# Optimization experiments

Hardware: AMD Instinct MI355X
Metric: run time of the kernel (lower is better)

## Reference

```python
import jax, jax.numpy as jnp
import numpy as np

R = 10000   # relation_num
E = 256     # emb_size == hidden_size
B = 1024    # batch
L = 8       # body length (loop runs L-1 steps)


def setup_inputs() -> dict:
    key = jax.random.key(0)
    ks = jax.random.split(key, 10)
    s = 0.05
    return {
        "bodys": jax.random.randint(ks[0], (B, L), 0, R),
        "emb_w": jax.random.normal(ks[1], (R, E), jnp.float32) * s,
        "w_ih": jax.random.normal(ks[2], (4 * E, E), jnp.float32) * s,
        "w_hh": jax.random.normal(ks[3], (4 * E, E), jnp.float32) * s,
        "b_ih": jax.random.normal(ks[4], (4 * E,), jnp.float32) * s,
        "b_hh": jax.random.normal(ks[5], (4 * E,), jnp.float32) * s,
        "fc1_w": jax.random.normal(ks[6], (E, 2 * E), jnp.float32) * s,
        "fc1_b": jax.random.normal(ks[7], (E,), jnp.float32) * s,
        "fc2_w": jax.random.normal(ks[8], (R + 1, E), jnp.float32) * s,
        "fc2_b": jax.random.normal(ks[9], (R + 1,), jnp.float32) * s,
    }


def _lstm(x, w_ih, w_hh, b_ih, b_hh):
    # x: [B, L, E] -> hidden states [B, L, H] (torch gate order i,f,g,o)
    Bn, _, H = x.shape[0], x.shape[1], w_hh.shape[1]
    h0 = jnp.zeros((Bn, H), x.dtype)
    c0 = jnp.zeros((Bn, H), x.dtype)

    def step(carry, xt):
        h, c = carry
        g = xt @ w_ih.T + b_ih + h @ w_hh.T + b_hh
        i, f, gg, o = jnp.split(g, 4, axis=-1)
        c = jax.nn.sigmoid(f) * c + jax.nn.sigmoid(i) * jnp.tanh(gg)
        h = jax.nn.sigmoid(o) * jnp.tanh(c)
        return (h, c), h

    _, hs = jax.lax.scan(step, (h0, c0), x.transpose(1, 0, 2))
    return hs.transpose(1, 0, 2)


def reference(bodys, emb_w, w_ih, w_hh, b_ih, b_hh, fc1_w, fc1_b, fc2_w, fc2_b):
    x = emb_w[bodys]                       # [B, L, E] embedded body relations
    body_hid = _lstm(x, w_ih, w_hh, b_ih, b_hh)  # [B, L, E]
    Rn = emb_w.shape[0]
    prob = emb_concat = prob_sf = None
    for i in range(body_hid.shape[1] - 1):   # short fixed unroll (L-1 steps)
        if i == 0:
            emb_1 = x[:, 0, :]
            second = x[:, 1, :]
        else:
            # prob_sf @ cat(embedding(indices), body_hid[:, i])  without [B,R+1,E]
            emb_1 = prob_sf[:, :Rn] @ emb_w + prob_sf[:, Rn:] * body_hid[:, i, :]
            # relation_emb[:, i+1, :] == emb_w[i+1] broadcast over batch
            second = jnp.broadcast_to(emb_w[i + 1], emb_1.shape)
        emb_concat = jnp.concatenate([emb_1, second], axis=1)   # [B, 2E]
        prob = jax.nn.relu(emb_concat @ fc1_w.T + fc1_b) @ fc2_w.T + fc2_b  # [B, R+1]
        prob_sf = jax.nn.softmax(prob, axis=1)
    return prob, emb_concat
```

## Files before the change

kernel.cpp:

```cpp
#include <hip/hip_runtime.h>

#define Bv 1024
#define Ev 256
#define Lv 8
#define Rv 10000
#define NP1 10001
#define PS2 10240
#define NPAD 10112
#define BM 64
#define BN 128
#define NSLICE 32
#define NSLOT 158
#define RPSTRIDE 160

typedef __attribute__((ext_vector_type(8))) short bf16x8;
typedef __attribute__((ext_vector_type(4))) float f32x4;

__device__ __forceinline__ float b2f(unsigned short u) {
    union { unsigned int i; float f; } v; v.i = ((unsigned int)u) << 16; return v.f;
}
__device__ __forceinline__ unsigned short f2b(float f) {
    union { float f; unsigned int i; } v; v.f = f;
    unsigned int r = v.i + 0x7fffu + ((v.i >> 16) & 1u);
    return (unsigned short)(r >> 16);
}
__device__ __forceinline__ void glds16(const void* g, void* l) {
    __builtin_amdgcn_global_load_lds(
        (const __attribute__((address_space(1))) void*)g,
        (__attribute__((address_space(3))) void*)l, 16, 0, 0);
}

__global__ __launch_bounds__(256) void gemm_tile(
    const unsigned short* __restrict__ A1, int lda1,
    const unsigned short* __restrict__ W1, int ldw1,
    const float* __restrict__ bias1,
    int Ktot, int kchunk, int Ncols, int mode,
    float* __restrict__ outF, unsigned short* __restrict__ outB, int ldc,
    float* __restrict__ rowPart, float* __restrict__ sfLastU)
{
    __shared__ unsigned short As[2][BM * 32];
    __shared__ unsigned short Bs[2][BN * 32];

    int bmode = mode & 7;
    int swz   = mode >> 4;
    int bx, by, bz;
    if (swz == 1) {
        int r = blockIdx.x & 7, q = blockIdx.x >> 3;
        bx = q & 15; by = r + (q >> 4) * 8; bz = 0;
        if (by >= NPAD / BN) return;
    } else if (swz == 2) {
        int r = blockIdx.x & 7, q = blockIdx.x >> 3;
        bz = r + (q >> 5) * 8; bx = (q & 31) >> 1; by = q & 1;
    } else {
        bx = blockIdx.x; by = blockIdx.y; bz = blockIdx.z;
    }

    int tid  = threadIdx.x;
    int wave = tid >> 6;
    int lane = tid & 63;
    int quad = lane >> 4;
    int l16  = lane & 15;
    int wm = (wave & 1) * 32;
    int wn = (wave >> 1) * 64;
    int m0 = bx * BM;
    int n0 = by * BN;
    int k0 = bz * kchunk;
    int k1 = k0 + kchunk; if (k1 > Ktot) k1 = Ktot;

    f32x4 acc[2][4];
#pragma unroll
    for (int i = 0; i < 2; ++i)
#pragma unroll
        for (int j = 0; j < 4; ++j) acc[i][j] = (f32x4){0.f, 0.f, 0.f, 0.f};

    int c0 = tid, c1 = 256 + tid;
    int row0 = c0 >> 2, row1 = c1 >> 2;
    int g80 = ((c0 & 3) ^ (row0 & 3) ^ ((row0 >> 2) & 3)) * 8;
    int g81 = ((c1 & 3) ^ (row1 & 3) ^ ((row1 >> 2) & 3)) * 8;

    bool first = true;
    for (int k = k0; k < k1; k += 64) {
        if (!first) __syncthreads();
        first = false;
#pragma unroll
        for (int h = 0; h < 2; ++h) {
            int kk = k + h * 32;
            glds16(A1 + (size_t)(m0 + row0) * lda1 + kk + g80, As[h] + (wave * 64) * 8);
            glds16(W1 + (size_t)(n0 + row0) * ldw1 + kk + g80, Bs[h] + (wave * 64) * 8);
            glds16(W1 + (size_t)(n0 + row1) * ldw1 + kk + g81, Bs[h] + (256 + wave * 64) * 8);
        }
        asm volatile("s_waitcnt vmcnt(0)" ::: "memory");
        __syncthreads();

#pragma unroll
        for (int h = 0; h < 2; ++h) {
            bf16x8 af[2], bfr[4];
#pragma unroll
            for (int t = 0; t < 2; ++t) {
                int m = wm + t * 16 + l16;
                int ca = quad ^ (m & 3) ^ ((m >> 2) & 3);
                af[t] = *(const bf16x8*)(As[h] + m * 32 + ca * 8);
            }
#pragma unroll
            for (int t = 0; t < 4; ++t) {
                int n = wn + t * 16 + l16;
                int cb = quad ^ (n & 3) ^ ((n >> 2) & 3);
                bfr[t] = *(const bf16x8*)(Bs[h] + n * 32 + cb * 8);
            }
#pragma unroll
            for (int i = 0; i < 2; ++i)
#pragma unroll
                for (int j = 0; j < 4; ++j)
                    acc[i][j] = __builtin_amdgcn_mfma_f32_16x16x32_bf16(
                        af[i], bfr[j], acc[i][j], 0, 0, 0);
        }
    }

    if (bmode == 5) {
        float rsum[2][4];
#pragma unroll
        for (int i = 0; i < 2; ++i)
#pragma unroll
            for (int r = 0; r < 4; ++r) rsum[i][r] = 0.f;
#pragma unroll
        for (int j = 0; j < 4; ++j) {
            int n = n0 + wn + j * 16 + l16;
            bool valid = (n < Ncols);
            float bsum = valid ? bias1[n] : 0.f;
#pragma unroll
            for (int i = 0; i < 2; ++i) {
                int mBase = m0 + wm + i * 16 + quad * 4;
#pragma unroll
                for (int r = 0; r < 4; ++r) {
                    float e = 0.f;
                    unsigned short w = 0;
                    if (valid) {
                        e = expf(acc[i][j][r] + bsum);
                        w = f2b(e);
                        if (n == Rv) sfLastU[mBase + r] = e;
                    }
                    outB[(size_t)(mBase + r) * ldc + n] = w;
                    rsum[i][r] += e;
                }
            }
        }
        int slot = by * 2 + (wn >> 6);
#pragma unroll
        for (int i = 0; i < 2; ++i)
#pragma unroll
            for (int r = 0; r < 4; ++r) {
                float s = rsum[i][r];
                s += __shfl_xor(s, 1);
                s += __shfl_xor(s, 2);
                s += __shfl_xor(s, 4);
                s += __shfl_xor(s, 8);
                if (l16 == 0) {
                    int m = m0 + wm + i * 16 + quad * 4 + r;
                    rowPart[(size_t)m * RPSTRIDE + slot] = s;
                }
            }
        return;
    }

#pragma unroll
    for (int j = 0; j < 4; ++j) {
        int n = n0 + wn + j * 16 + l16;
        if (n >= Ncols) continue;
        float bsum = bias1 ? bias1[n] : 0.f;
#pragma unroll
        for (int i = 0; i < 2; ++i) {
            int mBase = m0 + wm + i * 16 + quad * 4;
#pragma unroll
            for (int r = 0; r < 4; ++r) {
                float v = acc[i][j][r] + bsum;
                size_t idx = (size_t)(mBase + r) * ldc + n;
                if (bmode == 0)      outF[idx] = v;
                else                 outB[(size_t)bz * (Bv * Ev) + idx] = f2b(v);
            }
        }
    }
}

__global__ __launch_bounds__(256) void gemm64(
    const unsigned short* __restrict__ A1, int lda1,
    const unsigned short* __restrict__ W1, int ldw1,
    const float* __restrict__ bias1,
    int Ktot, int Ncols, int mode,
    float* __restrict__ outF, unsigned short* __restrict__ outB,
    int ldc, int nshift,
    const float* __restrict__ xgate, int tstep)
{
    __shared__ unsigned short As[2][64 * 32];
    __shared__ unsigned short Bs[2][64 * 32];

    int bmode = mode & 7;
    int bx = blockIdx.x >> nshift;
    int by = blockIdx.x & ((1 << nshift) - 1);
    int tid  = threadIdx.x;
    int wave = tid >> 6;
    int lane = tid & 63;
    int quad = lane >> 4;
    int l16  = lane & 15;
    int m0 = bx * 64;
    int n0 = by * 64;

    f32x4 acc[4];
#pragma unroll
    for (int j = 0; j < 4; ++j) acc[j] = (f32x4){0.f, 0.f, 0.f, 0.f};

    int row = tid >> 2;
    int g8  = ((tid & 3) ^ (row & 3) ^ ((row >> 2) & 3)) * 8;

    bool first = true;
    for (int k = 0; k < Ktot; k += 64) {
        if (!first) __syncthreads();
        first = false;
#pragma unroll
        for (int h = 0; h < 2; ++h) {
            int kk = k + h * 32;
            glds16(A1 + (size_t)(m0 + row) * lda1 + kk + g8, As[h] + wave * 512);
            glds16(W1 + (size_t)(n0 + row) * ldw1 + kk + g8, Bs[h] + wave * 512);
        }
        asm volatile("s_waitcnt vmcnt(0)" ::: "memory");
        __syncthreads();

#pragma unroll
        for (int h = 0; h < 2; ++h) {
            int ml = wave * 16 + l16;
            int ca = quad ^ (ml & 3) ^ ((ml >> 2) & 3);
            bf16x8 a = *(const bf16x8*)(As[h] + ml * 32 + ca * 8);
#pragma unroll
            for (int j = 0; j < 4; ++j) {
                int nl = j * 16 + l16;
                int cb = quad ^ (nl & 3) ^ ((nl >> 2) & 3);
                bf16x8 b = *(const bf16x8*)(Bs[h] + nl * 32 + cb * 8);
                acc[j] = __builtin_amdgcn_mfma_f32_16x16x32_bf16(a, b, acc[j], 0, 0, 0);
            }
        }
    }

    if (bmode == 4) {
        int e  = by * 16 + l16;
        float bi = bias1[n0 + l16];
        float bf_ = bias1[n0 + 16 + l16];
        float bg = bias1[n0 + 32 + l16];
        float bo = bias1[n0 + 48 + l16];
#pragma unroll
        for (int r = 0; r < 4; ++r) {
            int m = m0 + wave * 16 + quad * 4 + r;
            const float* xr = xgate + ((size_t)m * Lv + tstep) * 1024 + n0 + l16;
            float gi = acc[0][r] + bi + xr[0];
            float gf = acc[1][r] + bf_ + xr[16];
            float gg = acc[2][r] + bg + xr[32];
            float go = acc[3][r] + bo + xr[48];
            float cp = (mode & 8) ? 0.f : outF[(size_t)m * 256 + e];
            float si = 1.f / (1.f + expf(-gi));
            float sf = 1.f / (1.f + expf(-gf));
            float so = 1.f / (1.f + expf(-go));
            float cn = sf * cp + si * tanhf(gg);
            outF[(size_t)m * 256 + e] = cn;
            outB[(size_t)m * 256 + e] = f2b(so * tanhf(cn));
        }
        return;
    }

#pragma unroll
    for (int j = 0; j < 4; ++j) {
        int n = n0 + j * 16 + l16;
        if (n >= Ncols) continue;
        float bsum = bias1 ? bias1[n] : 0.f;
#pragma unroll
        for (int r = 0; r < 4; ++r) {
            int m = m0 + wave * 16 + quad * 4 + r;
            float v = acc[j][r] + bsum;
            if (bmode == 1) outB[(size_t)m * ldc + n] = f2b(v > 0.f ? v : 0.f);
            else            outB[(size_t)m * ldc + n] = f2b(v);
        }
    }
}

__global__ void prep_k(const float* __restrict__ w_ih,
                       const float* __restrict__ w_hh,
                       const float* __restrict__ fc1_w,
                       const float* __restrict__ fc2_w,
                       const float* __restrict__ b_ih,
                       const float* __restrict__ b_hh,
                       const int* __restrict__ bodys,
                       const float* __restrict__ emb_w,
                       const float* __restrict__ fc1_b,
                       unsigned short* __restrict__ w_ih_b,
                       unsigned short* __restrict__ w_hh_b,
                       unsigned short* __restrict__ fc1_w_b,
                       unsigned short* __restrict__ fc2_w_b,
                       float* __restrict__ biasC,
                       unsigned short* __restrict__ x,
                       unsigned short* __restrict__ embT,
                       unsigned short* __restrict__ embc,
                       unsigned short* __restrict__ sfA,
                       float* __restrict__ B2)
{
    __shared__ float tile[32][33];
    int b = blockIdx.x, t = threadIdx.x;
    if (b < 1264) {
#pragma unroll
        for (int j = 0; j < 8; ++j) {
            int i = b * 2048 + j * 256 + t;
            fc2_w_b[i] = (i < NP1 * Ev) ? f2b(fc2_w[i]) : (unsigned short)0;
        }
    } else if (b < 1520) {
        int bb = b - 1264;
        const float* src = (bb < 128) ? w_ih : w_hh;
        unsigned short* dst = (bb < 128) ? w_ih_b : w_hh_b;
        int rb = (bb & 127) * 8;
#pragma unroll
        for (int j = 0; j < 8; ++j) {
            int r = rb + j;
            int gate = (r >> 4) & 3;
            int e = (r & 15) | ((r >> 6) << 4);
            dst[(size_t)r * 256 + t] = f2b(src[(size_t)(gate * 256 + e) * 256 + t]);
        }
    } else if (b < 1584) {
        int base = (b - 1520) * 2048;
#pragma unroll
        for (int j = 0; j < 8; ++j) {
            int i = base + j * 256 + t;
            fc1_w_b[i] = f2b(fc1_w[i]);
        }
    } else if (b < 1585) {
#pragma unroll
        for (int j = 0; j < 4; ++j) {
            int r = j * 256 + t;
            int gate = (r >> 4) & 3;
            int e = (r & 15) | ((r >> 6) << 4);
            biasC[r] = b_ih[gate * 256 + e] + b_hh[gate * 256 + e];
        }
    } else if (b < 2609) {
        int bb = b - 1585;
#pragma unroll
        for (int j = 0; j < 8; ++j) {
            int row = bb * 8 + j;
            x[(size_t)row * Ev + t] = f2b(emb_w[(size_t)bodys[row] * Ev + t]);
        }
    } else if (b < 5169) {
        int bb = b - 2609;
        int kt = (bb % 320) * 32, et = (bb / 320) * 32;
        int tx = t & 31, ty = t >> 5;
#pragma unroll
        for (int r = ty; r < 32; r += 8) {
            int k = kt + r;
            tile[r][tx] = (k < Rv) ? emb_w[(size_t)k * Ev + et + tx] : 0.f;
        }
        __syncthreads();
#pragma unroll
        for (int r = ty; r < 32; r += 8) {
            embT[(size_t)(et + r) * PS2 + kt + tx] = f2b(tile[tx][r]);
        }
    } else if (b < 6193) {
        int bb = b - 5169;
        embc[(size_t)bb * 512 + t]       = f2b(emb_w[(size_t)bodys[bb * Lv + 0] * Ev + t]);
        embc[(size_t)bb * 512 + 256 + t] = f2b(emb_w[(size_t)bodys[bb * Lv + 1] * Ev + t]);
        if (t < PS2 - NPAD) sfA[(size_t)bb * PS2 + NPAD + t] = 0;
    } else {
        int i = b - 6193;
        const float* er = emb_w + (size_t)(i + 1) * Ev;
        const float* wr = fc1_w + (size_t)t * 512 + 256;
        float s = fc1_b[t];
        for (int k = 0; k < 256; ++k) s += wr[k] * er[k];
        B2[i * 256 + t] = s;
    }
}

__global__ void finalize_emb(const unsigned short* __restrict__ emb1p,
                             const float* __restrict__ rowPart,
                             const float* __restrict__ sfLastU,
                             const unsigned short* __restrict__ h_i,
                             const float* __restrict__ emb_row,
                             unsigned short* __restrict__ embc,
                             float* __restrict__ outTail)
{
    int b = blockIdx.x, e = threadIdx.x;
    int wave = e >> 6, lane = e & 63;
    __shared__ float sred[4];
    float ps = (e < NSLOT) ? rowPart[(size_t)b * RPSTRIDE + e] : 0.f;
    for (int off = 32; off; off >>= 1) ps += __shfl_down(ps, off);
    if (lane == 0) sred[wave] = ps;
    __syncthreads();
    float inv = 1.f / (sred[0] + sred[1] + sred[2] + sred[3]);

    float v = 0.f;
#pragma unroll
    for (int z = 0; z < NSLICE; ++z)
        v += b2f(emb1p[(size_t)z * (Bv * Ev) + (size_t)b * Ev + e]);
    v += sfLastU[b] * b2f(h_i[(size_t)b * Ev + e]);
    v *= inv;
    embc[(size_t)b * 512 + e] = f2b(v);
    if (outTail) {
        float w = emb_row[e];
        embc[(size_t)b * 512 + 256 + e]    = f2b(w);
        outTail[(size_t)b * 512 + e]       = v;
        outTail[(size_t)b * 512 + 256 + e] = w;
    }
}

extern "C" void kernel_launch(void* const* d_in, const int* in_sizes, int n_in,
                              void* d_out, int out_size, void* d_ws, size_t ws_size,
                              hipStream_t stream)
{
    const int*   bodys = (const int*)d_in[0];
    const float* emb_w = (const float*)d_in[1];
    const float* w_ih  = (const float*)d_in[2];
    const float* w_hh  = (const float*)d_in[3];
    const float* b_ih  = (const float*)d_in[4];
    const float* b_hh  = (const float*)d_in[5];
    const float* fc1_w = (const float*)d_in[6];
    const float* fc1_b = (const float*)d_in[7];
    const float* fc2_w = (const float*)d_in[8];
    const float* fc2_b = (const float*)d_in[9];
    float* out = (float*)d_out;

    char* ws = (char*)d_ws;
    size_t off = 0;
    auto alloc = [&](size_t bytes) -> void* {
        void* p = ws + off;
        off += (bytes + 255) & ~(size_t)255;
        return p;
    };
    unsigned short* x       = (unsigned short*)alloc((size_t)Bv * Lv * Ev * 2);
    unsigned short* hs      = (unsigned short*)alloc((size_t)Lv * Bv * Ev * 2);
    float*          cbuf    = (float*)alloc((size_t)Bv * Ev * 4);
    float*          xg      = (float*)alloc((size_t)Bv * Lv * 1024 * 4);
    unsigned short* embT    = (unsigned short*)alloc((size_t)Ev * PS2 * 2);
    unsigned short* sfA     = (unsigned short*)alloc((size_t)Bv * PS2 * 2);
    float*          sfLastU = (float*)alloc((size_t)Bv * 4);
    float*          rowPart = (float*)alloc((size_t)Bv * RPSTRIDE * 4);
    unsigned short* emb1p   = (unsigned short*)alloc((size_t)NSLICE * Bv * Ev * 2);
    unsigned short* embc    = (unsigned short*)alloc((size_t)Bv * 512 * 2);
    unsigned short* hiddenA = (unsigned short*)alloc((size_t)Bv * Ev * 2);
    unsigned short* w_ih_b  = (unsigned short*)alloc((size_t)1024 * Ev * 2);
    unsigned short* w_hh_b  = (unsigned short*)alloc((size_t)1024 * Ev * 2);
    float*          biasC   = (float*)alloc((size_t)1024 * 4);
    float*          B2      = (float*)alloc((size_t)7 * 256 * 4);
    unsigned short* fc1_w_b = (unsigned short*)alloc((size_t)Ev * 512 * 2);
    unsigned short* fc2_w_b = (unsigned short*)alloc((size_t)NPAD * Ev * 2);
    (void)ws_size; (void)in_sizes; (void)n_in; (void)out_size;

    prep_k<<<6200, 256, 0, stream>>>(w_ih, w_hh, fc1_w, fc2_w, b_ih, b_hh,
                                     bodys, emb_w, fc1_b,
                                     w_ih_b, w_hh_b, fc1_w_b, fc2_w_b, biasC, x,
                                     embT, embc, sfA, B2);

    gemm_tile<<<dim3(128, 8, 1), 256, 0, stream>>>(
        x, Ev, w_ih_b, Ev,
        nullptr,
        Ev, Ev, 1024, 0,
        xg, nullptr, 1024, nullptr, nullptr);

    for (int t = 0; t < Lv; ++t) {
        gemm64<<<256, 256, 0, stream>>>(
            hs + (size_t)(t ? t - 1 : 0) * Bv * Ev, Ev, w_hh_b, Ev,
            biasC,
            (t == 0) ? 0 : Ev, 1024, 4 | (t == 0 ? 8 : 0),
            cbuf, hs + (size_t)t * Bv * Ev, 1024, 4,
            xg, t);
    }

    for (int i = 0; i < 7; ++i) {
        if (i > 0) {
            gemm_tile<<<1024, 256, 0, stream>>>(
                sfA, PS2, embT, PS2,
                nullptr,
                PS2, PS2 / NSLICE, Ev, 2 | (2 << 4),
                nullptr, emb1p, Ev, nullptr, nullptr);
            finalize_emb<<<Bv, 256, 0, stream>>>(
                emb1p, rowPart, sfLastU, hs + (size_t)i * Bv * Ev,
                emb_w + (size_t)(i + 1) * Ev, embc,
                (i == 6) ? (out + (size_t)Bv * NP1) : nullptr);
        }
        if (i == 0) {
            gemm64<<<64, 256, 0, stream>>>(
                embc, 512, fc1_w_b, 512,
                fc1_b,
                512, 256, 1,
                nullptr, hiddenA, 256, 2,
                nullptr, 0);
        } else {
            gemm64<<<64, 256, 0, stream>>>(
                embc, 512, fc1_w_b, 512,
                B2 + (size_t)i * 256,
                256, 256, 1,
                nullptr, hiddenA, 256, 2,
                nullptr, 0);
        }
        if (i < 6) {
            gemm_tile<<<1280, 256, 0, stream>>>(
                hiddenA, Ev, fc2_w_b, Ev,
                fc2_b,
                Ev, Ev, NP1, 5 | (1 << 4),
                nullptr, sfA, PS2, rowPart, sfLastU);
        } else {
            gemm_tile<<<1280, 256, 0, stream>>>(
                hiddenA, Ev, fc2_w_b, Ev,
                fc2_b,
                Ev, Ev, NP1, 0 | (1 << 4),
                out, nullptr, NP1, nullptr, nullptr);
        }
    }
}
```

Measured before the change: 460.2 us.

## Fold fc1 into embedding table to fuse softmax-mix and fc1 layer

Precomputes EW1T = fc1_w[:, :E] @ emb_w^T and HW = hs @ fc1_w[:, :E]^T, so middle steps compute the fc1 pre-activation directly from the softmax-weighted sum, and finalize_emb applies bias and relu to write hiddenA. This removes the per-step fc1 gemm64 launch and reduces the split-K slice count from 32 to 16, halving the partial buffer traffic. The last step still uses the original embedding path to produce emb_concat output. It adds an up-front GEMM over the relation table plus extra prep work and memory, and rounding happens at a different point in bf16.

```diff
diff --git a/kernel.cpp b/kernel.cpp
--- a/kernel.cpp
+++ b/kernel.cpp
@@ -9,7 +9,7 @@
 #define NPAD 10112
 #define BM 64
 #define BN 128
-#define NSLICE 32
+#define NSLICE 16
 #define NSLOT 158
 #define RPSTRIDE 160
 
@@ -165,8 +165,9 @@
 #pragma unroll
     for (int j = 0; j < 4; ++j) {
         int n = n0 + wn + j * 16 + l16;
-        if (n >= Ncols) continue;
-        float bsum = bias1 ? bias1[n] : 0.f;
+        bool valid = (n < Ncols);
+        if (!valid && bmode != 3) continue;
+        float bsum = (valid && bias1) ? bias1[n] : 0.f;
 #pragma unroll
         for (int i = 0; i < 2; ++i) {
             int mBase = m0 + wm + i * 16 + quad * 4;
@@ -175,6 +176,7 @@
                 float v = acc[i][j][r] + bsum;
                 size_t idx = (size_t)(mBase + r) * ldc + n;
                 if (bmode == 0)      outF[idx] = v;
+                else if (bmode == 3) outB[idx] = valid ? f2b(v) : (unsigned short)0;
                 else                 outB[(size_t)bz * (Bv * Ev) + idx] = f2b(v);
             }
         }
@@ -297,7 +299,9 @@
                        unsigned short* __restrict__ embT,
                        unsigned short* __restrict__ embc,
                        unsigned short* __restrict__ sfA,
-                       float* __restrict__ B2)
+                       float* __restrict__ B2,
+                       unsigned short* __restrict__ emb_w_b,
+                       unsigned short* __restrict__ EW1T)
 {
     __shared__ float tile[32][33];
     int b = blockIdx.x, t = threadIdx.x;
@@ -360,13 +364,23 @@
         embc[(size_t)bb * 512 + t]       = f2b(emb_w[(size_t)bodys[bb * Lv + 0] * Ev + t]);
         embc[(size_t)bb * 512 + 256 + t] = f2b(emb_w[(size_t)bodys[bb * Lv + 1] * Ev + t]);
         if (t < PS2 - NPAD) sfA[(size_t)bb * PS2 + NPAD + t] = 0;
-    } else {
+    } else if (b < 6200) {
         int i = b - 6193;
         const float* er = emb_w + (size_t)(i + 1) * Ev;
         const float* wr = fc1_w + (size_t)t * 512 + 256;
         float s = fc1_b[t];
         for (int k = 0; k < 256; ++k) s += wr[k] * er[k];
         B2[i * 256 + t] = s;
+    } else if (b < 7464) {
+        int bb = b - 6200;
+#pragma unroll
+        for (int j = 0; j < 8; ++j) {
+            int i = bb * 2048 + j * 256 + t;
+            emb_w_b[i] = ((i >> 8) < Rv) ? f2b(emb_w[i]) : (unsigned short)0;
+        }
+    } else {
+        int idx = (b - 7464) * 256 + t;
+        EW1T[(size_t)(idx >> 7) * PS2 + NPAD + (idx & 127)] = 0;
     }
 }
 
@@ -376,7 +390,10 @@
                              const unsigned short* __restrict__ h_i,
                              const float* __restrict__ emb_row,
                              unsigned short* __restrict__ embc,
-                             float* __restrict__ outTail)
+                             float* __restrict__ outTail,
+                             const float* __restrict__ HWrow,
+                             const float* __restrict__ B2row,
+                             unsigned short* __restrict__ hiddenA)
 {
     int b = blockIdx.x, e = threadIdx.x;
     int wave = e >> 6, lane = e & 63;
@@ -387,14 +404,17 @@
     __syncthreads();
     float inv = 1.f / (sred[0] + sred[1] + sred[2] + sred[3]);
 
-    float v = 0.f;
+    float x1 = 0.f;
 #pragma unroll
     for (int z = 0; z < NSLICE; ++z)
-        v += b2f(emb1p[(size_t)z * (Bv * Ev) + (size_t)b * Ev + e]);
-    v += sfLastU[b] * b2f(h_i[(size_t)b * Ev + e]);
-    v *= inv;
-    embc[(size_t)b * 512 + e] = f2b(v);
-    if (outTail) {
+        x1 += b2f(emb1p[(size_t)z * (Bv * Ev) + (size_t)b * Ev + e]);
+
+    if (HWrow) {
+        float v = x1 * inv + sfLastU[b] * inv * HWrow[(size_t)b * 256 + e] + B2row[e];
+        hiddenA[(size_t)b * 256 + e] = f2b(v > 0.f ? v : 0.f);
+    } else {
+        float v = (x1 + sfLastU[b] * b2f(h_i[(size_t)b * Ev + e])) * inv;
+        embc[(size_t)b * 512 + e] = f2b(v);
         float w = emb_row[e];
         embc[(size_t)b * 512 + 256 + e]    = f2b(w);
         outTail[(size_t)b * 512 + e]       = v;
@@ -442,12 +462,28 @@
     float*          B2      = (float*)alloc((size_t)7 * 256 * 4);
     unsigned short* fc1_w_b = (unsigned short*)alloc((size_t)Ev * 512 * 2);
     unsigned short* fc2_w_b = (unsigned short*)alloc((size_t)NPAD * Ev * 2);
+    unsigned short* emb_w_b = (unsigned short*)alloc((size_t)NPAD * Ev * 2);
+    unsigned short* EW1T    = (unsigned short*)alloc((size_t)Ev * PS2 * 2);
+    float*          HW      = (float*)alloc((size_t)Lv * Bv * Ev * 4);
     (void)ws_size; (void)in_sizes; (void)n_in; (void)out_size;
 
-    prep_k<<<6200, 256, 0, stream>>>(w_ih, w_hh, fc1_w, fc2_w, b_ih, b_hh,
+    prep_k<<<7592, 256, 0, stream>>>(w_ih, w_hh, fc1_w, fc2_w, b_ih, b_hh,
                                      bodys, emb_w, fc1_b,
                                      w_ih_b, w_hh_b, fc1_w_b, fc2_w_b, biasC, x,
-                                     embT, embc, sfA, B2);
+                                     embT, embc, sfA, B2, emb_w_b, EW1T);
+
+    gemm_tile<<<dim3(4, 79, 1), 256, 0, stream>>>(
+        fc1_w_b, 512, emb_w_b, Ev,
+        nullptr,
+        Ev, Ev, Rv, 3,
+        nullptr, EW1T, PS2, nullptr, nullptr);
+
+    gemm64<<<64, 256, 0, stream>>>(
+        embc, 512, fc1_w_b, 512,
+        fc1_b,
+        512, 256, 1,
+        nullptr, hiddenA, 256, 2,
+        nullptr, 0);
 
     gemm_tile<<<dim3(128, 8, 1), 256, 0, stream>>>(
         x, Ev, w_ih_b, Ev,
@@ -464,32 +500,35 @@
             xg, t);
     }
 
+    gemm_tile<<<dim3(128, 2, 1), 256, 0, stream>>>(
+        hs, Ev, fc1_w_b, 512,
+        nullptr,
+        Ev, Ev, Ev, 0,
+        HW, nullptr, Ev, nullptr, nullptr);
+
     for (int i = 0; i < 7; ++i) {
         if (i > 0) {
-            gemm_tile<<<1024, 256, 0, stream>>>(
-                sfA, PS2, embT, PS2,
+            bool last = (i == 6);
+            gemm_tile<<<512, 256, 0, stream>>>(
+                sfA, PS2, last ? embT : EW1T, PS2,
                 nullptr,
                 PS2, PS2 / NSLICE, Ev, 2 | (2 << 4),
                 nullptr, emb1p, Ev, nullptr, nullptr);
             finalize_emb<<<Bv, 256, 0, stream>>>(
-                emb1p, rowPart, sfLastU, hs + (size_t)i * Bv * Ev,
-                emb_w + (size_t)(i + 1) * Ev, embc,
-                (i == 6) ? (out + (size_t)Bv * NP1) : nullptr);
-        }
-        if (i == 0) {
-            gemm64<<<64, 256, 0, stream>>>(
-                embc, 512, fc1_w_b, 512,
-                fc1_b,
-                512, 256, 1,
-                nullptr, hiddenA, 256, 2,
-                nullptr, 0);
-        } else {
-            gemm64<<<64, 256, 0, stream>>>(
-                embc, 512, fc1_w_b, 512,
-                B2 + (size_t)i * 256,
-                256, 256, 1,
-                nullptr, hiddenA, 256, 2,
-                nullptr, 0);
+                emb1p, rowPart, sfLastU,
+                hs + (size_t)i * Bv * Ev, emb_w + (size_t)(i + 1) * Ev,
+                embc, out + (size_t)Bv * NP1,
+                last ? nullptr : (HW + (size_t)i * Bv * Ev),
+                last ? nullptr : (B2 + (size_t)i * 256),
+                hiddenA);
+            if (last) {
+                gemm64<<<64, 256, 0, stream>>>(
+                    embc, 512, fc1_w_b, 512,
+                    B2 + (size_t)6 * 256,
+                    256, 256, 1,
+                    nullptr, hiddenA, 256, 2,
+                    nullptr, 0);
+            }
         }
         if (i < 6) {
             gemm_tile<<<1280, 256, 0, stream>>>(
```

Result: no change. 452.7 us (-1.6%).
